# Performance work log

Measured on AMD Instinct MI355X. Metric: run time of the kernel, lower is better.

Reference implementation:

```python
import jax, jax.numpy as jnp
import numpy as np

HEADS = 16
LN_EPS = 1e-5

def setup_inputs() -> dict:
    key = jax.random.key(0)
    ks = jax.random.split(key, 8)
    B, S, NT = 4, 1024, 1024
    sc = 1.0 / np.sqrt(NT)
    return {
        "x": jax.random.normal(ks[0], (B, S, NT), dtype=jnp.float32),
        "Wq": jax.random.normal(ks[1], (NT, NT), dtype=jnp.float32) * sc,
        "bq": jax.random.normal(ks[2], (NT,), dtype=jnp.float32) * 0.02,
        "Wk": jax.random.normal(ks[3], (NT, NT), dtype=jnp.float32) * sc,
        "bk": jax.random.normal(ks[4], (NT,), dtype=jnp.float32) * 0.02,
        "Wv": jax.random.normal(ks[5], (NT, NT), dtype=jnp.float32) * sc,
        "bv": jax.random.normal(ks[6], (NT,), dtype=jnp.float32) * 0.02,
        "gamma": jnp.ones((NT,), dtype=jnp.float32),
        "beta": jnp.zeros((NT,), dtype=jnp.float32),
    }

def reference(x, Wq, bq, Wk, bk, Wv, bv, gamma, beta):
    B, S, nt = x.shape
    heads = HEADS
    dph = nt // heads
    # torch nn.Linear: y = x @ W.T + b
    q = x @ Wq.T + bq
    k = x @ Wk.T + bk
    v = x @ Wv.T + bv
    # torch .view(B*heads, -1, dph) is a row-major reshape (interleaved split)
    q = q.reshape(B * heads, -1, dph)
    k = k.reshape(B * heads, -1, dph)
    v = v.reshape(B * heads, -1, dph)
    # scaled scores; scale uses last dim of the score matrix (== seq len here)
    att = jnp.einsum('bid,bjd->bij', q, k)
    scale = att.shape[-1] ** (-0.5)
    att = jax.nn.softmax(jax.nn.relu(att * scale), axis=-1)
    # dropout in eval mode -> identity
    at_sum_sum = att.sum(axis=1).reshape(B, heads, -1)  # [B, heads, S]
    context = jnp.einsum('bij,bjd->bid', att, v).reshape(B, -1, nt)
    h = x + context
    mu = h.mean(axis=-1, keepdims=True)
    var = h.var(axis=-1, keepdims=True)
    out = (h - mu) * jax.lax.rsqrt(var + LN_EPS) * gamma + beta
    return out, at_sum_sum
```

## Files before the change

kernel.cpp:

```cpp
#include <hip/hip_runtime.h>
#include <hip/hip_bf16.h>
#include <cstdint>
#include <cstddef>


typedef short short8 __attribute__((ext_vector_type(8)));
typedef short short4v __attribute__((ext_vector_type(4)));
typedef float f32x4 __attribute__((ext_vector_type(4)));

#define MFMA32(a, b, c) __builtin_amdgcn_mfma_f32_16x16x32_bf16(a, b, c, 0, 0, 0)
#define MFMA16x16(a, b, c) __builtin_amdgcn_mfma_f32_16x16x16bf16_1k(a, b, c, 0, 0, 0)
#define ATT_SCALE 0.03125f

__device__ __forceinline__ short f2bf(float f) {
  union { float f; uint32_t u; } x; x.f = f;
  uint32_t u = x.u + 0x7fffu + ((x.u >> 16) & 1u);
  return (short)(u >> 16);
}

__device__ __forceinline__ uint32_t pk_bf16_trunc(float lo, float hi) {
  return __builtin_amdgcn_perm(__float_as_uint(hi), __float_as_uint(lo),
                               0x07060302u);
}

#define GLDS16(gp, lp)                                                        \
  __builtin_amdgcn_global_load_lds(                                           \
      (const __attribute__((address_space(1))) void*)(gp),                    \
      (__attribute__((address_space(3))) void*)(lp), 16, 0, 0)
#define GLDS4(gp, lp)                                                         \
  __builtin_amdgcn_global_load_lds(                                           \
      (const __attribute__((address_space(1))) void*)(gp),                    \
      (__attribute__((address_space(3))) void*)(lp), 4, 0, 0)

__global__ __launch_bounds__(256) void convert_kernel(
    const float* __restrict__ x, const float* __restrict__ wq,
    const float* __restrict__ wk, const float* __restrict__ wv,
    short* __restrict__ xb, short* __restrict__ wb) {
  const long XN = 4L * 1024 * 1024, WN = 1024L * 1024;
  long e = (long)(blockIdx.x * blockDim.x + threadIdx.x) * 4;
  const float* src; short* dst;
  if (e < XN)               { src = x  + e;                dst = xb + e; }
  else if (e < XN + WN)     { src = wq + (e - XN);         dst = wb + (e - XN); }
  else if (e < XN + 2 * WN) { src = wk + (e - XN - WN);    dst = wb + (e - XN); }
  else                      { src = wv + (e - XN - 2*WN);  dst = wb + (e - XN); }
  f32x4 v = *(const f32x4*)src;
  short4v o;
  o[0] = f2bf(v[0]); o[1] = f2bf(v[1]); o[2] = f2bf(v[2]); o[3] = f2bf(v[3]);
  *(short4v*)dst = o;
}

__global__ __launch_bounds__(256, 3) void qkv_gemm(
    const short* __restrict__ xb, const short* __restrict__ wb,
    const float* __restrict__ bq, const float* __restrict__ bk,
    const float* __restrict__ bv, short* __restrict__ qb,
    short* __restrict__ kb, short* __restrict__ vtp) {
  __shared__ short As[128 * 32];
  __shared__ short Bs[128 * 32];
  const int tid = threadIdx.x;
  const int lane = tid & 63;
  const int lm = lane & 15, quad = lane >> 4;
  const int wave = tid >> 6, wy = wave >> 1, wx = wave & 1;
  const int m0 = blockIdx.y * 128, n0 = blockIdx.x * 128;
  const int z = blockIdx.z;
  const short* w = wb + (size_t)z * (1024 * 1024);
  const float* bias = (z == 0) ? bq : (z == 1) ? bk : bv;
  const float scl = (z == 0) ? ATT_SCALE : 1.0f;

  const short* gA0 = xb + (size_t)(m0 + (tid >> 2)) * 1024 + (tid & 3) * 8;
  const short* gA1 = gA0 + 64 * 1024;
  const short* gB0 = w  + (size_t)(n0 + (tid >> 2)) * 1024 + (tid & 3) * 8;
  const short* gB1 = gB0 + 64 * 1024;
  short* lA0 = As + tid * 8;
  short* lA1 = As + (tid + 256) * 8;
  short* lB0 = Bs + tid * 8;
  short* lB1 = Bs + (tid + 256) * 8;

  f32x4 acc[4][4];
#pragma unroll
  for (int i = 0; i < 4; i++)
#pragma unroll
    for (int j = 0; j < 4; j++) acc[i][j] = (f32x4){0.f, 0.f, 0.f, 0.f};

  for (int k0 = 0; k0 < 1024; k0 += 32) {
    GLDS16(gA0 + k0, lA0);
    GLDS16(gA1 + k0, lA1);
    GLDS16(gB0 + k0, lB0);
    GLDS16(gB1 + k0, lB1);
    __syncthreads();
    short8 a[4], b[4];
#pragma unroll
    for (int t = 0; t < 4; t++)
      a[t] = *(const short8*)(As + (wy * 64 + t * 16 + lm) * 32 + quad * 8);
#pragma unroll
    for (int t = 0; t < 4; t++)
      b[t] = *(const short8*)(Bs + (wx * 64 + t * 16 + lm) * 32 + quad * 8);
#pragma unroll
    for (int mt = 0; mt < 4; mt++)
#pragma unroll
      for (int nt = 0; nt < 4; nt++)
        acc[mt][nt] = MFMA32(a[mt], b[nt], acc[mt][nt]);
    __syncthreads();
  }
  if (z == 2) {
#pragma unroll
    for (int nt = 0; nt < 4; nt++) {
      const int n = n0 + wx * 64 + nt * 16 + lm;
      const float bn = bias[n];
      const size_t nbase = (size_t)((n >> 4) & 3) * 16384 +
                           (size_t)((((n >> 8) & 3) * 16 + (n & 15)) * 4 +
                                    ((n >> 6) & 3));
#pragma unroll
      for (int mt = 0; mt < 4; mt++) {
#pragma unroll
        for (int r = 0; r < 4; r++) {
          const int m = m0 + wy * 64 + mt * 16 + quad * 4 + r;
          vtp[(size_t)(m >> 6) * 65536 + nbase + (size_t)(m & 63) * 256] =
              f2bf(acc[mt][nt][r] + bn);
        }
      }
    }
  } else {
    short* out = (z == 0) ? qb : kb;
#pragma unroll
    for (int nt = 0; nt < 4; nt++) {
      const int n = n0 + wx * 64 + nt * 16 + lm;
      const float bn = bias[n];
#pragma unroll
      for (int mt = 0; mt < 4; mt++) {
        const int mb = m0 + wy * 64 + mt * 16 + quad * 4;
#pragma unroll
        for (int r = 0; r < 4; r++)
          out[(size_t)(mb + r) * 1024 + n] = f2bf((acc[mt][nt][r] + bn) * scl);
      }
    }
  }
}

__global__ __launch_bounds__(256, 2) void attn_kernel(
    const short* __restrict__ qb, const short* __restrict__ kb,
    const short* __restrict__ vtp, const float* __restrict__ x,
    const float* __restrict__ gamma, const float* __restrict__ beta,
    float* __restrict__ out1, float* __restrict__ rvW) {
  __shared__ short Ks[2][64 * 64];
  __shared__ short Vs[2][4 * 4 * 256];

  const int tid = threadIdx.x;
  const int lane = tid & 63, wave = tid >> 6;
  const int lm = lane & 15, quad = lane >> 4;
  const int h = blockIdx.x >> 3, bb = blockIdx.x & 7;
  const short* Qh = qb + (size_t)h * 65536;
  const short* Kh = kb + (size_t)h * 65536;
  const short* Vp = vtp + (size_t)h * 65536;
  const int i0 = bb * 128 + wave * 32;

  const short8 qA0 = *(const short8*)(Qh + (size_t)(i0 + lm) * 64 + quad * 8);
  const short8 qA1 = *(const short8*)(Qh + (size_t)(i0 + lm) * 64 + 32 + quad * 8);
  const short8 qB0 = *(const short8*)(Qh + (size_t)(i0 + 16 + lm) * 64 + quad * 8);
  const short8 qB1 = *(const short8*)(Qh + (size_t)(i0 + 16 + lm) * 64 + 32 + quad * 8);

  const int c0 = tid, c1 = tid + 256;
  const short* gK0 = Kh + (size_t)(c0 >> 3) * 64 + ((c0 & 7) ^ ((c0 >> 3) & 7)) * 8;
  const short* gK1 = Kh + (size_t)(c1 >> 3) * 64 + ((c1 & 7) ^ ((c1 >> 3) & 7)) * 8;
  const short* gV0 = Vp + (c0 >> 7) * 16384 + ((c0 >> 5) & 3) * 256 + (c0 & 31) * 8;
  const short* gV1 = Vp + (c1 >> 7) * 16384 + ((c1 >> 5) & 3) * 256 + (c1 & 31) * 8;
  const int lK0 = c0 * 8, lK1 = c1 * 8;

  f32x4 accA[4], accB[4];
#pragma unroll
  for (int t = 0; t < 4; t++) {
    accA[t] = (f32x4){0.f, 0.f, 0.f, 0.f};
    accB[t] = (f32x4){0.f, 0.f, 0.f, 0.f};
  }
  float dsA[4] = {0.f, 0.f, 0.f, 0.f};
  float dsB[4] = {0.f, 0.f, 0.f, 0.f};

  const int swz0 = (quad ^ (lm & 7)) * 8;
  const int swz1 = ((quad + 4) ^ (lm & 7)) * 8;

  GLDS16(gK0, &Ks[0][0] + lK0);
  GLDS16(gK1, &Ks[0][0] + lK1);
  GLDS16(gV0, &Vs[0][0] + lK0);
  GLDS16(gV1, &Vs[0][0] + lK1);

  for (int ch = 0; ch < 16; ch++) {
    const int b = ch & 1;
    __syncthreads();
    if (ch < 15) {
      const int ko = (ch + 1) * 4096, vo = (ch + 1) * 1024;
      GLDS16(gK0 + ko, &Ks[b ^ 1][0] + lK0);
      GLDS16(gK1 + ko, &Ks[b ^ 1][0] + lK1);
      GLDS16(gV0 + vo, &Vs[b ^ 1][0] + lK0);
      GLDS16(gV1 + vo, &Vs[b ^ 1][0] + lK1);
    }
#pragma unroll
    for (int jj = 0; jj < 4; jj++) {
      const short* krow = &Ks[b][(jj * 16 + lm) * 64];
      const short8 kf0 = *(const short8*)(krow + swz0);
      const short8 kf1 = *(const short8*)(krow + swz1);
      f32x4 zA = {0.f, 0.f, 0.f, 0.f};
      zA = MFMA32(kf0, qA0, zA);
      zA = MFMA32(kf1, qA1, zA);
      f32x4 zB = {0.f, 0.f, 0.f, 0.f};
      zB = MFMA32(kf0, qB0, zB);
      zB = MFMA32(kf1, qB1, zB);
      float pA[4], pB[4];
#pragma unroll
      for (int r = 0; r < 4; r++) {
        pA[r] = __expf(fmaxf(zA[r], 0.f));
        dsA[r] += pA[r];
        pB[r] = __expf(fmaxf(zB[r], 0.f));
        dsB[r] += pB[r];
      }
      union { uint32_t u[2]; short4v s; } puA, puB;
      puA.u[0] = pk_bf16_trunc(pA[0], pA[1]);
      puA.u[1] = pk_bf16_trunc(pA[2], pA[3]);
      puB.u[0] = pk_bf16_trunc(pB[0], pB[1]);
      puB.u[1] = pk_bf16_trunc(pB[2], pB[3]);
      const short* vbase = &Vs[b][jj * 256 + lane * 4];
#pragma unroll
      for (int dt = 0; dt < 4; dt++) {
        const short4v vtf = *(const short4v*)(vbase + dt * 1024);
        accA[dt] = MFMA16x16(vtf, puA.s, accA[dt]);
        accB[dt] = MFMA16x16(vtf, puB.s, accB[dt]);
      }
    }
  }
  float tA = (dsA[0] + dsA[1]) + (dsA[2] + dsA[3]);
  tA += __shfl_xor(tA, 16);
  tA += __shfl_xor(tA, 32);
  float tB = (dsB[0] + dsB[1]) + (dsB[2] + dsB[3]);
  tB += __shfl_xor(tB, 16);
  tB += __shfl_xor(tB, 32);
  const float rvA = 1.f / tA;
  const float rvB = 1.f / tB;
  if (lane < 16) {
    rvW[h * 1024 + i0 + lm] = rvA;
    rvW[h * 1024 + i0 + 16 + lm] = rvB;
  }

  const int mA = h * 64 + bb * 8 + wave * 2;
  const int nb = lm * 64 + quad * 4;
#pragma unroll
  for (int tile = 0; tile < 2; tile++) {
    const int m = mA + tile;
    const f32x4* accT = tile ? accB : accA;
    const float rv = tile ? rvB : rvA;
    const float* xr = x + (size_t)m * 1024;
    float hv[4][4], s1 = 0.f, s2 = 0.f;
#pragma unroll
    for (int dt = 0; dt < 4; dt++) {
      f32x4 xv = *(const f32x4*)(xr + nb + dt * 16);
#pragma unroll
      for (int r = 0; r < 4; r++) {
        const float v = xv[r] + accT[dt][r] * rv;
        hv[dt][r] = v; s1 += v; s2 += v * v;
      }
    }
#pragma unroll
    for (int mk = 1; mk < 64; mk <<= 1) {
      s1 += __shfl_xor(s1, mk);
      s2 += __shfl_xor(s2, mk);
    }
    const float mu = s1 * (1.f / 1024.f);
    const float var = s2 * (1.f / 1024.f) - mu * mu;
    const float rstd = rsqrtf(var + 1e-5f);
    float* orow = out1 + (size_t)m * 1024;
#pragma unroll
    for (int dt = 0; dt < 4; dt++) {
      f32x4 gv = *(const f32x4*)(gamma + nb + dt * 16);
      f32x4 bv2 = *(const f32x4*)(beta + nb + dt * 16);
      f32x4 ov;
#pragma unroll
      for (int r = 0; r < 4; r++)
        ov[r] = (hv[dt][r] - mu) * rstd * gv[r] + bv2[r];
      *(f32x4*)(orow + nb + dt * 16) = ov;
    }
  }
}

__global__ __launch_bounds__(256, 2) void colsum_kernel(
    const short* __restrict__ qb, const short* __restrict__ kb,
    const float* __restrict__ rvW, float* __restrict__ out2) {
  __shared__ short Qs[2][64 * 64];
  __shared__ float rvS[2][64];

  const int tid = threadIdx.x;
  const int lane = tid & 63, wave = tid >> 6;
  const int lm = lane & 15, quad = lane >> 4;
  const int h = blockIdx.x >> 3, jb = blockIdx.x & 7;
  const int j0 = jb * 128 + wave * 32;
  const short* Qh = qb + (size_t)h * 65536;
  const short* Kh = kb + (size_t)h * 65536;
  const float* rvh = rvW + h * 1024;

  const short* krA = Kh + (size_t)(j0 + lm) * 64 + quad * 8;
  const short8 kA0 = *(const short8*)krA;
  const short8 kA1 = *(const short8*)(krA + 32);
  const short* krB = Kh + (size_t)(j0 + 16 + lm) * 64 + quad * 8;
  const short8 kB0 = *(const short8*)krB;
  const short8 kB1 = *(const short8*)(krB + 32);

  const int c0 = tid, c1 = tid + 256;
  const short* gQ0 = Qh + (size_t)(c0 >> 3) * 64 + ((c0 & 7) ^ ((c0 >> 3) & 7)) * 8;
  const short* gQ1 = Qh + (size_t)(c1 >> 3) * 64 + ((c1 & 7) ^ ((c1 >> 3) & 7)) * 8;
  const int lQ0 = c0 * 8, lQ1 = c1 * 8;

  const int swz0 = (quad ^ (lm & 7)) * 8;
  const int swz1 = ((quad + 4) ^ (lm & 7)) * 8;

  f32x4 csA = {0.f, 0.f, 0.f, 0.f};
  f32x4 csB = {0.f, 0.f, 0.f, 0.f};

  GLDS16(gQ0, &Qs[0][0] + lQ0);
  GLDS16(gQ1, &Qs[0][0] + lQ1);
  if (wave == 0) GLDS4(rvh + lane, &rvS[0][0]);

  for (int ch = 0; ch < 16; ch++) {
    const int b = ch & 1;
    __syncthreads();
    if (ch < 15) {
      const int qo = (ch + 1) * 4096;
      GLDS16(gQ0 + qo, &Qs[b ^ 1][0] + lQ0);
      GLDS16(gQ1 + qo, &Qs[b ^ 1][0] + lQ1);
      if (wave == 0) GLDS4(rvh + (ch + 1) * 64 + lane, &rvS[b ^ 1][0]);
    }
#pragma unroll
    for (int ii = 0; ii < 4; ii++) {
      const short* qrow = &Qs[b][(ii * 16 + lm) * 64];
      const short8 qf0 = *(const short8*)(qrow + swz0);
      const short8 qf1 = *(const short8*)(qrow + swz1);
      f32x4 zA = {0.f, 0.f, 0.f, 0.f};
      zA = MFMA32(kA0, qf0, zA);
      zA = MFMA32(kA1, qf1, zA);
      f32x4 zB = {0.f, 0.f, 0.f, 0.f};
      zB = MFMA32(kB0, qf0, zB);
      zB = MFMA32(kB1, qf1, zB);
      const float rvv = rvS[b][ii * 16 + lm];
#pragma unroll
      for (int r = 0; r < 4; r++) {
        csA[r] += __expf(fmaxf(zA[r], 0.f)) * rvv;
        csB[r] += __expf(fmaxf(zB[r], 0.f)) * rvv;
      }
    }
  }
#pragma unroll
  for (int mk = 1; mk < 16; mk <<= 1)
#pragma unroll
    for (int r = 0; r < 4; r++) {
      csA[r] += __shfl_xor(csA[r], mk);
      csB[r] += __shfl_xor(csB[r], mk);
    }
  if (lm == 0) {
    *(f32x4*)(out2 + h * 1024 + j0 + quad * 4) = csA;
    *(f32x4*)(out2 + h * 1024 + j0 + 16 + quad * 4) = csB;
  }
}

extern "C" void kernel_launch(void* const* d_in, const int* in_sizes, int n_in,
                              void* d_out, int out_size, void* d_ws, size_t ws_size,
                              hipStream_t stream) {
  const float* x  = (const float*)d_in[0];
  const float* Wq = (const float*)d_in[1];
  const float* bq = (const float*)d_in[2];
  const float* Wk = (const float*)d_in[3];
  const float* bk = (const float*)d_in[4];
  const float* Wv = (const float*)d_in[5];
  const float* bv = (const float*)d_in[6];
  const float* gamma = (const float*)d_in[7];
  const float* beta  = (const float*)d_in[8];

  float* out1 = (float*)d_out;
  float* out2 = out1 + 4L * 1024 * 1024;

  short* xb = (short*)d_ws;
  short* wb = xb + 4L * 1024 * 1024;
  short* qb = wb + 3L * 1024 * 1024;
  short* kb = qb + 4L * 1024 * 1024;
  short* vtp = kb + 4L * 1024 * 1024;
  float* rvW = (float*)wb;

  convert_kernel<<<7168, 256, 0, stream>>>(x, Wq, Wk, Wv, xb, wb);
  qkv_gemm<<<dim3(8, 32, 3), 256, 0, stream>>>(xb, wb, bq, bk, bv, qb, kb, vtp);
  attn_kernel<<<512, 256, 0, stream>>>(qb, kb, vtp, x, gamma, beta, out1, rvW);
  colsum_kernel<<<512, 256, 0, stream>>>(qb, kb, rvW, out2);
}
```

Before: 181.8 us.

## Triple-buffer attention and colsum loads, and remap block indices for locality

The attention and colsum loops move from double to triple buffering of the LDS tiles. Each iteration now waits with an explicit vmcnt count plus a raw barrier, and the prefetch two chunks ahead is issued after the compute, so load latency overlaps more compute. Block indices in the QKV GEMM and in both attention kernels are remapped so that concurrently running blocks share heads or tiles, which should improve cache and XCD locality. The change uses more LDS per block, relies on exact counts of outstanding memory operations (hence the dummy wrap-around load and every wave doing the rv load), and may lower occupancy.

Result: faster. 168.9 us (-7.1%).

```diff
diff --git a/kernel.cpp b/kernel.cpp
--- a/kernel.cpp
+++ b/kernel.cpp
@@ -60,7 +60,10 @@
   const int lane = tid & 63;
   const int lm = lane & 15, quad = lane >> 4;
   const int wave = tid >> 6, wy = wave >> 1, wx = wave & 1;
-  const int m0 = blockIdx.y * 128, n0 = blockIdx.x * 128;
+  const int f = blockIdx.x + (blockIdx.y << 3);
+  const int r8 = f & 7, s = f >> 3;
+  const int m0 = (((r8 >> 1) << 3) + (s & 7)) * 128;
+  const int n0 = (((r8 & 1) << 2) + (s >> 3)) * 128;
   const int z = blockIdx.z;
   const short* w = wb + (size_t)z * (1024 * 1024);
   const float* bias = (z == 0) ? bq : (z == 1) ? bk : bv;
@@ -141,13 +144,15 @@
     const short* __restrict__ vtp, const float* __restrict__ x,
     const float* __restrict__ gamma, const float* __restrict__ beta,
     float* __restrict__ out1, float* __restrict__ rvW) {
-  __shared__ short Ks[2][64 * 64];
-  __shared__ short Vs[2][4 * 4 * 256];
+  __shared__ short Ks[3][64 * 64];
+  __shared__ short Vs[3][4 * 4 * 256];
 
   const int tid = threadIdx.x;
   const int lane = tid & 63, wave = tid >> 6;
   const int lm = lane & 15, quad = lane >> 4;
-  const int h = blockIdx.x >> 3, bb = blockIdx.x & 7;
+  const int bid = blockIdx.x;
+  const int h = ((bid >> 6) << 3) + (bid & 7);
+  const int bb = (bid >> 3) & 7;
   const short* Qh = qb + (size_t)h * 65536;
   const short* Kh = kb + (size_t)h * 65536;
   const short* Vp = vtp + (size_t)h * 65536;
@@ -165,6 +170,15 @@
   const short* gV1 = Vp + (c1 >> 7) * 16384 + ((c1 >> 5) & 3) * 256 + (c1 & 31) * 8;
   const int lK0 = c0 * 8, lK1 = c1 * 8;
 
+#define ATTN_STAGE(c, buf)                                                    \
+  do {                                                                        \
+    const int ko_ = ((c) & 15) * 4096, vo_ = ((c) & 15) * 1024;               \
+    GLDS16(gK0 + ko_, &Ks[buf][0] + lK0);                                     \
+    GLDS16(gK1 + ko_, &Ks[buf][0] + lK1);                                     \
+    GLDS16(gV0 + vo_, &Vs[buf][0] + lK0);                                     \
+    GLDS16(gV1 + vo_, &Vs[buf][0] + lK1);                                     \
+  } while (0)
+
   f32x4 accA[4], accB[4];
 #pragma unroll
   for (int t = 0; t < 4; t++) {
@@ -177,21 +191,13 @@
   const int swz0 = (quad ^ (lm & 7)) * 8;
   const int swz1 = ((quad + 4) ^ (lm & 7)) * 8;
 
-  GLDS16(gK0, &Ks[0][0] + lK0);
-  GLDS16(gK1, &Ks[0][0] + lK1);
-  GLDS16(gV0, &Vs[0][0] + lK0);
-  GLDS16(gV1, &Vs[0][0] + lK1);
+  ATTN_STAGE(0, 0);
+  ATTN_STAGE(1, 1);
 
   for (int ch = 0; ch < 16; ch++) {
-    const int b = ch & 1;
-    __syncthreads();
-    if (ch < 15) {
-      const int ko = (ch + 1) * 4096, vo = (ch + 1) * 1024;
-      GLDS16(gK0 + ko, &Ks[b ^ 1][0] + lK0);
-      GLDS16(gK1 + ko, &Ks[b ^ 1][0] + lK1);
-      GLDS16(gV0 + vo, &Vs[b ^ 1][0] + lK0);
-      GLDS16(gV1 + vo, &Vs[b ^ 1][0] + lK1);
-    }
+    const int b = ch % 3, bs = (ch + 2) % 3;
+    asm volatile("s_waitcnt vmcnt(4)" ::: "memory");
+    __builtin_amdgcn_s_barrier();
 #pragma unroll
     for (int jj = 0; jj < 4; jj++) {
       const short* krow = &Ks[b][(jj * 16 + lm) * 64];
@@ -224,7 +230,10 @@
         accB[dt] = MFMA16x16(vtf, puB.s, accB[dt]);
       }
     }
-  }
+    if (ch < 15) ATTN_STAGE(ch + 2, bs);
+  }
+  asm volatile("s_waitcnt vmcnt(0)" ::: "memory");
+
   float tA = (dsA[0] + dsA[1]) + (dsA[2] + dsA[3]);
   tA += __shfl_xor(tA, 16);
   tA += __shfl_xor(tA, 32);
@@ -281,13 +290,15 @@
 __global__ __launch_bounds__(256, 2) void colsum_kernel(
     const short* __restrict__ qb, const short* __restrict__ kb,
     const float* __restrict__ rvW, float* __restrict__ out2) {
-  __shared__ short Qs[2][64 * 64];
-  __shared__ float rvS[2][64];
+  __shared__ short Qs[3][64 * 64];
+  __shared__ float rvS[3][64];
 
   const int tid = threadIdx.x;
   const int lane = tid & 63, wave = tid >> 6;
   const int lm = lane & 15, quad = lane >> 4;
-  const int h = blockIdx.x >> 3, jb = blockIdx.x & 7;
+  const int bid = blockIdx.x;
+  const int h = ((bid >> 6) << 3) + (bid & 7);
+  const int jb = (bid >> 3) & 7;
   const int j0 = jb * 128 + wave * 32;
   const short* Qh = qb + (size_t)h * 65536;
   const short* Kh = kb + (size_t)h * 65536;
@@ -305,25 +316,27 @@
   const short* gQ1 = Qh + (size_t)(c1 >> 3) * 64 + ((c1 & 7) ^ ((c1 >> 3) & 7)) * 8;
   const int lQ0 = c0 * 8, lQ1 = c1 * 8;
 
+#define CS_STAGE(c, buf)                                                      \
+  do {                                                                        \
+    const int qo_ = ((c) & 15) * 4096;                                        \
+    GLDS16(gQ0 + qo_, &Qs[buf][0] + lQ0);                                     \
+    GLDS16(gQ1 + qo_, &Qs[buf][0] + lQ1);                                     \
+    GLDS4(rvh + ((c) & 15) * 64 + lane, &rvS[buf][0]);                        \
+  } while (0)
+
   const int swz0 = (quad ^ (lm & 7)) * 8;
   const int swz1 = ((quad + 4) ^ (lm & 7)) * 8;
 
   f32x4 csA = {0.f, 0.f, 0.f, 0.f};
   f32x4 csB = {0.f, 0.f, 0.f, 0.f};
 
-  GLDS16(gQ0, &Qs[0][0] + lQ0);
-  GLDS16(gQ1, &Qs[0][0] + lQ1);
-  if (wave == 0) GLDS4(rvh + lane, &rvS[0][0]);
+  CS_STAGE(0, 0);
+  CS_STAGE(1, 1);
 
   for (int ch = 0; ch < 16; ch++) {
-    const int b = ch & 1;
-    __syncthreads();
-    if (ch < 15) {
-      const int qo = (ch + 1) * 4096;
-      GLDS16(gQ0 + qo, &Qs[b ^ 1][0] + lQ0);
-      GLDS16(gQ1 + qo, &Qs[b ^ 1][0] + lQ1);
-      if (wave == 0) GLDS4(rvh + (ch + 1) * 64 + lane, &rvS[b ^ 1][0]);
-    }
+    const int b = ch % 3, bs = (ch + 2) % 3;
+    asm volatile("s_waitcnt vmcnt(3)" ::: "memory");
+    __builtin_amdgcn_s_barrier();
 #pragma unroll
     for (int ii = 0; ii < 4; ii++) {
       const short* qrow = &Qs[b][(ii * 16 + lm) * 64];
@@ -342,7 +355,10 @@
         csB[r] += __expf(fmaxf(zB[r], 0.f)) * rvv;
       }
     }
-  }
+    if (ch < 15) CS_STAGE(ch + 2, bs);
+  }
+  asm volatile("s_waitcnt vmcnt(0)" ::: "memory");
+
 #pragma unroll
   for (int mk = 1; mk < 16; mk <<= 1)
 #pragma unroll
```
